# Kernel optimization log

Measured on AMD Instinct MI355X. Metric: run time of the kernel, lower is better.

Reference implementation:

```python
import jax, jax.numpy as jnp
import numpy as np

B, T, D, H = 4, 2048, 512, 8
DH = D // H

def setup_inputs() -> dict:
    key = jax.random.key(0)
    k1, k2, k3, k4 = jax.random.split(key, 4)
    scale = 1.0 / np.sqrt(D)
    return {
        "x": jax.random.normal(k1, (B, T, D), dtype=jnp.float32),
        "attn_mask": jnp.ones((B, T), dtype=jnp.int32),
        "bias": jax.random.normal(k2, (B, T, T), dtype=jnp.float32),
        "W_qkv": jax.random.normal(k3, (D, 3 * D), dtype=jnp.float32) * scale,
        "W_out": jax.random.normal(k4, (D, D), dtype=jnp.float32) * scale,
    }

def reference(x, attn_mask, bias, W_qkv, W_out):
    qkv = x @ W_qkv                      # [B,T,3D]
    q, k, v = jnp.split(qkv, 3, axis=-1)
    def heads(t):                        # [B,T,D] -> [B,H,T,DH]
        return t.reshape(B, T, H, DH).transpose(0, 2, 1, 3)
    q, k, v = heads(q), heads(k), heads(v)
    logits = jnp.einsum('bhqd,bhkd->bhqk', q, k) / np.sqrt(DH)
    logits = logits + bias[:, None, :, :]
    mask = (attn_mask[:, None, None, :] != 0)
    logits = jnp.where(mask, logits, -jnp.inf)
    attn = jax.nn.softmax(logits, axis=-1)
    out = jnp.einsum('bhqk,bhkd->bhqd', attn, v)  # [B,H,T,DH]
    out = out.transpose(0, 2, 1, 3).reshape(B, T, D)
    return out @ W_out
```

## Files before the change

kernel.cpp:

```cpp
#include <hip/hip_runtime.h>
#include <hip/hip_bf16.h>
#include <stdint.h>

#define Bc 4
#define Tc 2048
#define Dc 512
#define Hc 8

typedef __bf16 bf16x8 __attribute__((ext_vector_type(8)));
typedef float  f32x4  __attribute__((ext_vector_type(4)));
typedef unsigned short u16x8 __attribute__((ext_vector_type(8)));

__device__ __forceinline__ unsigned short f2b(float f) {
  union { float f; unsigned u; } v; v.f = f;
  unsigned r = v.u + 0x7fffu + ((v.u >> 16) & 1u);
  return (unsigned short)(r >> 16);
}

__device__ __forceinline__ unsigned short f2b_native(float f) {
  __bf16 b = (__bf16)f;
  return __builtin_bit_cast(unsigned short, b);
}

__device__ __forceinline__ bf16x8 ld_frag(const unsigned short* p) {
  u16x8 u = *(const u16x8*)p;
  return __builtin_bit_cast(bf16x8, u);
}

__device__ __forceinline__ void gload_lds16(const unsigned short* g, unsigned short* l) {
  __builtin_amdgcn_global_load_lds((const __attribute__((address_space(1))) void*)g,
                                   (__attribute__((address_space(3))) void*)l,
                                   16, 0, 0);
}

__global__ __launch_bounds__(256) void cvt_bf16(const float* __restrict__ in,
                                                unsigned short* __restrict__ out, int n) {
  int i = (blockIdx.x * 256 + threadIdx.x) * 8;
  if (i >= n) return;
  float4 a = *(const float4*)&in[i];
  float4 b = *(const float4*)&in[i + 4];
  u16x8 r;
  r[0] = f2b(a.x); r[1] = f2b(a.y); r[2] = f2b(a.z); r[3] = f2b(a.w);
  r[4] = f2b(b.x); r[5] = f2b(b.y); r[6] = f2b(b.z); r[7] = f2b(b.w);
  *(u16x8*)&out[i] = r;
}

__global__ __launch_bounds__(256) void transp_bf16(const float* __restrict__ in,
                                                   unsigned short* __restrict__ out,
                                                   int R, int C) {
  __shared__ float tile[32][33];
  int c0 = blockIdx.x * 32, r0 = blockIdx.y * 32;
  int lx = threadIdx.x & 31, ly = threadIdx.x >> 5;
  #pragma unroll
  for (int i = 0; i < 32; i += 8) tile[ly + i][lx] = in[(size_t)(r0 + ly + i) * C + c0 + lx];
  __syncthreads();
  #pragma unroll
  for (int i = 0; i < 32; i += 8) out[(size_t)(c0 + ly + i) * R + r0 + lx] = f2b(tile[lx][ly + i]);
}

__global__ __launch_bounds__(256) void transp_v(const unsigned short* __restrict__ qkv,
                                                unsigned short* __restrict__ vtg) {
  __shared__ unsigned short tile[32][34];
  int t0 = blockIdx.x * 32;
  int d0 = blockIdx.y * 32;
  int b  = blockIdx.z;
  int lx = threadIdx.x & 31, ly = threadIdx.x >> 5;
  #pragma unroll
  for (int i = 0; i < 32; i += 8)
    tile[ly + i][lx] = qkv[(size_t)(b * Tc + t0 + ly + i) * 1536 + 1024 + d0 + lx];
  __syncthreads();
  #pragma unroll
  for (int i = 0; i < 32; i += 8)
    vtg[(size_t)(b * 512 + d0 + ly + i) * Tc + t0 + lx] = tile[lx][ly + i];
}

template <int N, int OUTF32>
__global__ __launch_bounds__(256) void gemm_bt(const unsigned short* __restrict__ A,
                                               const unsigned short* __restrict__ Bt,
                                               void* __restrict__ Cout, int M, int K) {
  __shared__ unsigned short As[128 * 32];
  __shared__ unsigned short Bs[128 * 32];
  const int tid = threadIdx.x;
  const int lane = tid & 63;
  const int wid = tid >> 6;
  const int wm = (wid >> 1) * 64;
  const int wn = (wid & 1) * 64;
  const int m0 = blockIdx.x * 128;
  const int n0 = blockIdx.y * 128;
  const int l15 = lane & 15;
  const int lg = lane >> 4;

  f32x4 acc[4][4];
  #pragma unroll
  for (int i = 0; i < 4; i++)
    #pragma unroll
    for (int j = 0; j < 4; j++) acc[i][j] = (f32x4){0.f, 0.f, 0.f, 0.f};

  const int srow = tid >> 2;
  const int scol = (tid & 3) * 8;

  for (int k0 = 0; k0 < K; k0 += 32) {
    __syncthreads();
    gload_lds16(&A[(size_t)(m0 + srow) * K + k0 + scol],      &As[tid * 8]);
    gload_lds16(&A[(size_t)(m0 + 64 + srow) * K + k0 + scol], &As[2048 + tid * 8]);
    gload_lds16(&Bt[(size_t)(n0 + srow) * K + k0 + scol],      &Bs[tid * 8]);
    gload_lds16(&Bt[(size_t)(n0 + 64 + srow) * K + k0 + scol], &Bs[2048 + tid * 8]);
    __syncthreads();
    bf16x8 af[4], bfr[4];
    #pragma unroll
    for (int m = 0; m < 4; m++) af[m] = ld_frag(&As[(wm + m * 16 + l15) * 32 + lg * 8]);
    #pragma unroll
    for (int n = 0; n < 4; n++) bfr[n] = ld_frag(&Bs[(wn + n * 16 + l15) * 32 + lg * 8]);
    #pragma unroll
    for (int m = 0; m < 4; m++)
      #pragma unroll
      for (int n = 0; n < 4; n++)
        acc[m][n] = __builtin_amdgcn_mfma_f32_16x16x32_bf16(af[m], bfr[n], acc[m][n], 0, 0, 0);
  }

  #pragma unroll
  for (int m = 0; m < 4; m++)
    #pragma unroll
    for (int n = 0; n < 4; n++)
      #pragma unroll
      for (int j = 0; j < 4; j++) {
        int row = m0 + wm + m * 16 + lg * 4 + j;
        int col = n0 + wn + n * 16 + l15;
        float v = acc[m][n][j];
        if (OUTF32) ((float*)Cout)[(size_t)row * N + col] = v;
        else ((unsigned short*)Cout)[(size_t)row * N + col] = f2b(v);
      }
}

__global__ __launch_bounds__(256, 5) void attn_kernel(const unsigned short* __restrict__ qkv,
                                                      const unsigned short* __restrict__ vtg,
                                                      const float* __restrict__ bias,
                                                      const int* __restrict__ amask,
                                                      unsigned short* __restrict__ ctx) {
  __shared__ unsigned short Ks[64 * 64];
  __shared__ unsigned short Vs[64 * 64];
  __shared__ unsigned short Pt[4][16 * 72];

  const int NQ = Tc / 64;
  const int bid = blockIdx.x;
  const int b = bid / (Hc * NQ);
  const int h = (bid / NQ) % Hc;
  const int q0 = (bid % NQ) * 64;
  const int tid = threadIdx.x;
  const int lane = tid & 63;
  const int w = tid >> 6;
  const int l15 = lane & 15;
  const int lg = lane >> 4;

  const float LOG2E = 1.44269504f;

  const int qrow = q0 + w * 16 + l15;
  const size_t qoff = (size_t)(b * Tc + qrow) * 1536 + h * 64;
  bf16x8 qf0 = ld_frag(&qkv[qoff + lg * 8]);
  bf16x8 qf1 = ld_frag(&qkv[qoff + 32 + lg * 8]);

  u16x8 ou;
  #pragma unroll
  for (int e = 0; e < 8; e++) ou[e] = 0x3f80;
  const bf16x8 ones = __builtin_bit_cast(bf16x8, ou);

  f32x4 o[4];
  f32x4 osum = (f32x4){0.f, 0.f, 0.f, 0.f};
  #pragma unroll
  for (int n = 0; n < 4; n++) o[n] = (f32x4){0.f, 0.f, 0.f, 0.f};

  const int skey = tid >> 3;
  const int sc = tid & 7;
  const int sgc = sc ^ (skey & 7);

  const size_t kcol = (size_t)b * Tc * 1536 + 512 + h * 64;
  const unsigned short* vrow = &vtg[(size_t)(b * 512 + h * 64) * Tc];

  const float* bq = bias + (size_t)(b * Tc + q0 + w * 16 + l15) * Tc;
  const int* mq = amask + b * Tc;

  unsigned short* ptw = &Pt[w][0];

  for (int kt = 0; kt < Tc; kt += 64) {
    __syncthreads();
    {
      const size_t kbase = kcol + (size_t)kt * 1536;
      gload_lds16(&qkv[kbase + (size_t)skey * 1536 + sgc * 8],        &Ks[tid * 8]);
      gload_lds16(&qkv[kbase + (size_t)(skey + 32) * 1536 + sgc * 8], &Ks[2048 + tid * 8]);
      gload_lds16(&vrow[(size_t)skey * Tc + kt + sgc * 8],        &Vs[tid * 8]);
      gload_lds16(&vrow[(size_t)(skey + 32) * Tc + kt + sgc * 8], &Vs[2048 + tid * 8]);
    }
    float bf_[4][4];
    #pragma unroll
    for (int t2 = 0; t2 < 4; t2++) {
      float4 bb = *(const float4*)&bq[kt + t2 * 16 + lg * 4];
      int4 mm = *(const int4*)&mq[kt + t2 * 16 + lg * 4];
      bf_[t2][0] = mm.x ? bb.x * LOG2E : -1e30f;
      bf_[t2][1] = mm.y ? bb.y * LOG2E : -1e30f;
      bf_[t2][2] = mm.z ? bb.z * LOG2E : -1e30f;
      bf_[t2][3] = mm.w ? bb.w * LOG2E : -1e30f;
    }
    __syncthreads();

    f32x4 s[4];
    #pragma unroll
    for (int t2 = 0; t2 < 4; t2++) {
      int key = t2 * 16 + l15;
      bf16x8 kb0 = ld_frag(&Ks[key * 64 + ((lg) ^ (key & 7)) * 8]);
      bf16x8 kb1 = ld_frag(&Ks[key * 64 + ((4 + lg) ^ (key & 7)) * 8]);
      f32x4 z = (f32x4){0.f, 0.f, 0.f, 0.f};
      z = __builtin_amdgcn_mfma_f32_16x16x32_bf16(kb0, qf0, z, 0, 0, 0);
      z = __builtin_amdgcn_mfma_f32_16x16x32_bf16(kb1, qf1, z, 0, 0, 0);
      s[t2] = z;
    }

    #pragma unroll
    for (int t2 = 0; t2 < 4; t2++)
      #pragma unroll
      for (int j = 0; j < 4; j++)
        s[t2][j] = exp2f(fmaf(s[t2][j], 0.125f * LOG2E, bf_[t2][j]));

    #pragma unroll
    for (int t2 = 0; t2 < 4; t2++) {
      ushort4 pw;
      pw.x = f2b_native(s[t2][0]);
      pw.y = f2b_native(s[t2][1]);
      pw.z = f2b_native(s[t2][2]);
      pw.w = f2b_native(s[t2][3]);
      *(ushort4*)&ptw[l15 * 72 + t2 * 16 + lg * 4] = pw;
    }

    #pragma unroll
    for (int ks = 0; ks < 2; ks++) {
      bf16x8 pa = ld_frag(&ptw[l15 * 72 + ks * 32 + lg * 8]);
      osum = __builtin_amdgcn_mfma_f32_16x16x32_bf16(pa, ones, osum, 0, 0, 0);
      #pragma unroll
      for (int n = 0; n < 4; n++) {
        int d = n * 16 + l15;
        bf16x8 vb = ld_frag(&Vs[d * 64 + ((ks * 4 + lg) ^ (d & 7)) * 8]);
        o[n] = __builtin_amdgcn_mfma_f32_16x16x32_bf16(pa, vb, o[n], 0, 0, 0);
      }
    }
  }

  #pragma unroll
  for (int n = 0; n < 4; n++)
    #pragma unroll
    for (int j = 0; j < 4; j++) {
      int q = q0 + w * 16 + lg * 4 + j;
      ctx[(size_t)(b * Tc + q) * Dc + h * 64 + n * 16 + l15] = f2b(o[n][j] / osum[j]);
    }
}

extern "C" void kernel_launch(void* const* d_in, const int* in_sizes, int n_in,
                              void* d_out, int out_size, void* d_ws, size_t ws_size,
                              hipStream_t stream) {
  const float* x     = (const float*)d_in[0];
  const int*   amask = (const int*)d_in[1];
  const float* bias  = (const float*)d_in[2];
  const float* Wqkv  = (const float*)d_in[3];
  const float* Wout  = (const float*)d_in[4];
  float* out = (float*)d_out;
  char* ws = (char*)d_ws;

  unsigned short* xb    = (unsigned short*)(ws + 0);
  unsigned short* wqkvT = (unsigned short*)(ws + 8388608);
  unsigned short* woutT = (unsigned short*)(ws + 9961472);
  unsigned short* qkv   = (unsigned short*)(ws + 10485760);
  unsigned short* ctx   = (unsigned short*)(ws + 35651584);
  unsigned short* vtg   = (unsigned short*)(ws + 44040192);

  cvt_bf16<<<2048, 256, 0, stream>>>(x, xb, Bc * Tc * Dc);
  transp_bf16<<<dim3(48, 16), 256, 0, stream>>>(Wqkv, wqkvT, 512, 1536);
  transp_bf16<<<dim3(16, 16), 256, 0, stream>>>(Wout, woutT, 512, 512);
  gemm_bt<1536, 0><<<dim3(64, 12), 256, 0, stream>>>(xb, wqkvT, (void*)qkv, 8192, 512);
  transp_v<<<dim3(64, 16, 4), 256, 0, stream>>>(qkv, vtg);
  attn_kernel<<<1024, 256, 0, stream>>>(qkv, vtg, bias, amask, ctx);
  gemm_bt<512, 1><<<dim3(64, 4), 256, 0, stream>>>(ctx, woutT, (void*)out, 8192, 512);
}
```

Baseline: 158.8 us.

## Process 32 query rows per wave to reuse K/V tiles across two groups

Each attention block now covers 128 query rows instead of 64. Each wave handles two 16-row groups that share the same K and V fragments loaded from LDS, so every K/V tile staged in shared memory feeds twice as many MFMAs and K/V global traffic is halved. The launch drops to 512 blocks, which is only about two blocks per CU on the MI355X. The occupancy hint is removed, and s_setprio is raised around the MFMA sections. The costs are more registers per thread and fewer waves available to hide latency.

```diff
diff --git a/kernel.cpp b/kernel.cpp
--- a/kernel.cpp
+++ b/kernel.cpp
@@ -132,20 +132,20 @@
       }
 }
 
-__global__ __launch_bounds__(256, 5) void attn_kernel(const unsigned short* __restrict__ qkv,
-                                                      const unsigned short* __restrict__ vtg,
-                                                      const float* __restrict__ bias,
-                                                      const int* __restrict__ amask,
-                                                      unsigned short* __restrict__ ctx) {
+__global__ __launch_bounds__(256) void attn_kernel(const unsigned short* __restrict__ qkv,
+                                                   const unsigned short* __restrict__ vtg,
+                                                   const float* __restrict__ bias,
+                                                   const int* __restrict__ amask,
+                                                   unsigned short* __restrict__ ctx) {
   __shared__ unsigned short Ks[64 * 64];
   __shared__ unsigned short Vs[64 * 64];
-  __shared__ unsigned short Pt[4][16 * 72];
-
-  const int NQ = Tc / 64;
+  __shared__ unsigned short Pt[4][32 * 78];
+
+  const int NQ = Tc / 128;
   const int bid = blockIdx.x;
   const int b = bid / (Hc * NQ);
   const int h = (bid / NQ) % Hc;
-  const int q0 = (bid % NQ) * 64;
+  const int q0 = (bid % NQ) * 128;
   const int tid = threadIdx.x;
   const int lane = tid & 63;
   const int w = tid >> 6;
@@ -153,21 +153,30 @@
   const int lg = lane >> 4;
 
   const float LOG2E = 1.44269504f;
-
-  const int qrow = q0 + w * 16 + l15;
-  const size_t qoff = (size_t)(b * Tc + qrow) * 1536 + h * 64;
-  bf16x8 qf0 = ld_frag(&qkv[qoff + lg * 8]);
-  bf16x8 qf1 = ld_frag(&qkv[qoff + 32 + lg * 8]);
+  const float SC = 0.125f * LOG2E;
+
+  bf16x8 qf[2][2];
+  #pragma unroll
+  for (int g = 0; g < 2; g++) {
+    const int qrow = q0 + w * 32 + g * 16 + l15;
+    const size_t qoff = (size_t)(b * Tc + qrow) * 1536 + h * 64;
+    qf[g][0] = ld_frag(&qkv[qoff + lg * 8]);
+    qf[g][1] = ld_frag(&qkv[qoff + 32 + lg * 8]);
+  }
 
   u16x8 ou;
   #pragma unroll
   for (int e = 0; e < 8; e++) ou[e] = 0x3f80;
   const bf16x8 ones = __builtin_bit_cast(bf16x8, ou);
 
-  f32x4 o[4];
-  f32x4 osum = (f32x4){0.f, 0.f, 0.f, 0.f};
-  #pragma unroll
-  for (int n = 0; n < 4; n++) o[n] = (f32x4){0.f, 0.f, 0.f, 0.f};
+  f32x4 o[2][4];
+  f32x4 osum[2];
+  #pragma unroll
+  for (int g = 0; g < 2; g++) {
+    osum[g] = (f32x4){0.f, 0.f, 0.f, 0.f};
+    #pragma unroll
+    for (int n = 0; n < 4; n++) o[g][n] = (f32x4){0.f, 0.f, 0.f, 0.f};
+  }
 
   const int skey = tid >> 3;
   const int sc = tid & 7;
@@ -176,7 +185,10 @@
   const size_t kcol = (size_t)b * Tc * 1536 + 512 + h * 64;
   const unsigned short* vrow = &vtg[(size_t)(b * 512 + h * 64) * Tc];
 
-  const float* bq = bias + (size_t)(b * Tc + q0 + w * 16 + l15) * Tc;
+  const float* bq[2];
+  #pragma unroll
+  for (int g = 0; g < 2; g++)
+    bq[g] = bias + (size_t)(b * Tc + q0 + w * 32 + g * 16 + l15) * Tc;
   const int* mq = amask + b * Tc;
 
   unsigned short* ptw = &Pt[w][0];
@@ -190,66 +202,85 @@
       gload_lds16(&vrow[(size_t)skey * Tc + kt + sgc * 8],        &Vs[tid * 8]);
       gload_lds16(&vrow[(size_t)(skey + 32) * Tc + kt + sgc * 8], &Vs[2048 + tid * 8]);
     }
-    float bf_[4][4];
+    float bf_[2][4][4];
     #pragma unroll
     for (int t2 = 0; t2 < 4; t2++) {
-      float4 bb = *(const float4*)&bq[kt + t2 * 16 + lg * 4];
       int4 mm = *(const int4*)&mq[kt + t2 * 16 + lg * 4];
-      bf_[t2][0] = mm.x ? bb.x * LOG2E : -1e30f;
-      bf_[t2][1] = mm.y ? bb.y * LOG2E : -1e30f;
-      bf_[t2][2] = mm.z ? bb.z * LOG2E : -1e30f;
-      bf_[t2][3] = mm.w ? bb.w * LOG2E : -1e30f;
+      float m0 = mm.x ? 0.f : -1e30f;
+      float m1 = mm.y ? 0.f : -1e30f;
+      float m2 = mm.z ? 0.f : -1e30f;
+      float m3 = mm.w ? 0.f : -1e30f;
+      #pragma unroll
+      for (int g = 0; g < 2; g++) {
+        float4 bb = *(const float4*)&bq[g][kt + t2 * 16 + lg * 4];
+        bf_[g][t2][0] = fmaf(bb.x, LOG2E, m0);
+        bf_[g][t2][1] = fmaf(bb.y, LOG2E, m1);
+        bf_[g][t2][2] = fmaf(bb.z, LOG2E, m2);
+        bf_[g][t2][3] = fmaf(bb.w, LOG2E, m3);
+      }
     }
     __syncthreads();
 
-    f32x4 s[4];
+    f32x4 s[2][4];
+    __builtin_amdgcn_s_setprio(1);
     #pragma unroll
     for (int t2 = 0; t2 < 4; t2++) {
-      int key = t2 * 16 + l15;
+      const int key = t2 * 16 + l15;
       bf16x8 kb0 = ld_frag(&Ks[key * 64 + ((lg) ^ (key & 7)) * 8]);
       bf16x8 kb1 = ld_frag(&Ks[key * 64 + ((4 + lg) ^ (key & 7)) * 8]);
-      f32x4 z = (f32x4){0.f, 0.f, 0.f, 0.f};
-      z = __builtin_amdgcn_mfma_f32_16x16x32_bf16(kb0, qf0, z, 0, 0, 0);
-      z = __builtin_amdgcn_mfma_f32_16x16x32_bf16(kb1, qf1, z, 0, 0, 0);
-      s[t2] = z;
-    }
-
-    #pragma unroll
-    for (int t2 = 0; t2 < 4; t2++)
-      #pragma unroll
-      for (int j = 0; j < 4; j++)
-        s[t2][j] = exp2f(fmaf(s[t2][j], 0.125f * LOG2E, bf_[t2][j]));
-
-    #pragma unroll
-    for (int t2 = 0; t2 < 4; t2++) {
-      ushort4 pw;
-      pw.x = f2b_native(s[t2][0]);
-      pw.y = f2b_native(s[t2][1]);
-      pw.z = f2b_native(s[t2][2]);
-      pw.w = f2b_native(s[t2][3]);
-      *(ushort4*)&ptw[l15 * 72 + t2 * 16 + lg * 4] = pw;
-    }
-
+      #pragma unroll
+      for (int g = 0; g < 2; g++) {
+        f32x4 z = (f32x4){0.f, 0.f, 0.f, 0.f};
+        z = __builtin_amdgcn_mfma_f32_16x16x32_bf16(kb0, qf[g][0], z, 0, 0, 0);
+        z = __builtin_amdgcn_mfma_f32_16x16x32_bf16(kb1, qf[g][1], z, 0, 0, 0);
+        s[g][t2] = z;
+      }
+    }
+    __builtin_amdgcn_s_setprio(0);
+
+    #pragma unroll
+    for (int g = 0; g < 2; g++) {
+      #pragma unroll
+      for (int t2 = 0; t2 < 4; t2++) {
+        #pragma unroll
+        for (int j = 0; j < 4; j++)
+          s[g][t2][j] = exp2f(fmaf(s[g][t2][j], SC, bf_[g][t2][j]));
+        ushort4 pw;
+        pw.x = f2b_native(s[g][t2][0]);
+        pw.y = f2b_native(s[g][t2][1]);
+        pw.z = f2b_native(s[g][t2][2]);
+        pw.w = f2b_native(s[g][t2][3]);
+        *(ushort4*)&ptw[(g * 16 + l15) * 78 + t2 * 16 + lg * 4] = pw;
+      }
+    }
+
+    __builtin_amdgcn_s_setprio(1);
     #pragma unroll
     for (int ks = 0; ks < 2; ks++) {
-      bf16x8 pa = ld_frag(&ptw[l15 * 72 + ks * 32 + lg * 8]);
-      osum = __builtin_amdgcn_mfma_f32_16x16x32_bf16(pa, ones, osum, 0, 0, 0);
+      bf16x8 pa0 = ld_frag(&ptw[(0 * 16 + l15) * 78 + ks * 32 + lg * 8]);
+      bf16x8 pa1 = ld_frag(&ptw[(1 * 16 + l15) * 78 + ks * 32 + lg * 8]);
+      osum[0] = __builtin_amdgcn_mfma_f32_16x16x32_bf16(pa0, ones, osum[0], 0, 0, 0);
+      osum[1] = __builtin_amdgcn_mfma_f32_16x16x32_bf16(pa1, ones, osum[1], 0, 0, 0);
       #pragma unroll
       for (int n = 0; n < 4; n++) {
-        int d = n * 16 + l15;
+        const int d = n * 16 + l15;
         bf16x8 vb = ld_frag(&Vs[d * 64 + ((ks * 4 + lg) ^ (d & 7)) * 8]);
-        o[n] = __builtin_amdgcn_mfma_f32_16x16x32_bf16(pa, vb, o[n], 0, 0, 0);
-      }
-    }
+        o[0][n] = __builtin_amdgcn_mfma_f32_16x16x32_bf16(pa0, vb, o[0][n], 0, 0, 0);
+        o[1][n] = __builtin_amdgcn_mfma_f32_16x16x32_bf16(pa1, vb, o[1][n], 0, 0, 0);
+      }
+    }
+    __builtin_amdgcn_s_setprio(0);
   }
 
   #pragma unroll
-  for (int n = 0; n < 4; n++)
-    #pragma unroll
-    for (int j = 0; j < 4; j++) {
-      int q = q0 + w * 16 + lg * 4 + j;
-      ctx[(size_t)(b * Tc + q) * Dc + h * 64 + n * 16 + l15] = f2b(o[n][j] / osum[j]);
-    }
+  for (int g = 0; g < 2; g++)
+    #pragma unroll
+    for (int n = 0; n < 4; n++)
+      #pragma unroll
+      for (int j = 0; j < 4; j++) {
+        int q = q0 + w * 32 + g * 16 + lg * 4 + j;
+        ctx[(size_t)(b * Tc + q) * Dc + h * 64 + n * 16 + l15] = f2b(o[g][n][j] / osum[g][j]);
+      }
 }
 
 extern "C" void kernel_launch(void* const* d_in, const int* in_sizes, int n_in,
@@ -275,6 +306,6 @@
   transp_bf16<<<dim3(16, 16), 256, 0, stream>>>(Wout, woutT, 512, 512);
   gemm_bt<1536, 0><<<dim3(64, 12), 256, 0, stream>>>(xb, wqkvT, (void*)qkv, 8192, 512);
   transp_v<<<dim3(64, 16, 4), 256, 0, stream>>>(qkv, vtg);
-  attn_kernel<<<1024, 256, 0, stream>>>(qkv, vtg, bias, amask, ctx);
+  attn_kernel<<<512, 256, 0, stream>>>(qkv, vtg, bias, amask, ctx);
   gemm_bt<512, 1><<<dim3(64, 4), 256, 0, stream>>>(ctx, woutT, (void*)out, 8192, 512);
 }
```

Measured after the change: 180.0 us. 13.3% more time.

## Swizzle P tile in LDS, pack bf16 converts, add MFMA priority hints

Applied to the files above, without the earlier changes.

The P staging buffer moves from a padded 72-stride layout to an XOR-swizzled 64-stride layout. This trims LDS use and avoids bank conflicts on the write and fragment-read paths. Float-to-bf16 conversion now uses the packed v_cvt_pk_bf16_f32 instruction, and s_setprio raises wave priority around the two MFMA phases. The min-blocks launch bound of 5 is dropped, which lets the compiler use more registers but may lower occupancy.

```diff
diff --git a/kernel.cpp b/kernel.cpp
--- a/kernel.cpp
+++ b/kernel.cpp
@@ -17,11 +17,6 @@
   return (unsigned short)(r >> 16);
 }
 
-__device__ __forceinline__ unsigned short f2b_native(float f) {
-  __bf16 b = (__bf16)f;
-  return __builtin_bit_cast(unsigned short, b);
-}
-
 __device__ __forceinline__ bf16x8 ld_frag(const unsigned short* p) {
   u16x8 u = *(const u16x8*)p;
   return __builtin_bit_cast(bf16x8, u);
@@ -31,6 +26,12 @@
   __builtin_amdgcn_global_load_lds((const __attribute__((address_space(1))) void*)g,
                                    (__attribute__((address_space(3))) void*)l,
                                    16, 0, 0);
+}
+
+__device__ __forceinline__ unsigned cvtpk_bf16(float lo, float hi) {
+  unsigned r;
+  asm("v_cvt_pk_bf16_f32 %0, %1, %2" : "=v"(r) : "v"(lo), "v"(hi));
+  return r;
 }
 
 __global__ __launch_bounds__(256) void cvt_bf16(const float* __restrict__ in,
@@ -132,14 +133,14 @@
       }
 }
 
-__global__ __launch_bounds__(256, 5) void attn_kernel(const unsigned short* __restrict__ qkv,
-                                                      const unsigned short* __restrict__ vtg,
-                                                      const float* __restrict__ bias,
-                                                      const int* __restrict__ amask,
-                                                      unsigned short* __restrict__ ctx) {
+__global__ __launch_bounds__(256) void attn_kernel(const unsigned short* __restrict__ qkv,
+                                                   const unsigned short* __restrict__ vtg,
+                                                   const float* __restrict__ bias,
+                                                   const int* __restrict__ amask,
+                                                   unsigned short* __restrict__ ctx) {
   __shared__ unsigned short Ks[64 * 64];
   __shared__ unsigned short Vs[64 * 64];
-  __shared__ unsigned short Pt[4][16 * 72];
+  __shared__ unsigned short Pt[4][16 * 64];
 
   const int NQ = Tc / 64;
   const int bid = blockIdx.x;
@@ -153,6 +154,7 @@
   const int lg = lane >> 4;
 
   const float LOG2E = 1.44269504f;
+  const float SC = 0.125f * LOG2E;
 
   const int qrow = q0 + w * 16 + l15;
   const size_t qoff = (size_t)(b * Tc + qrow) * 1536 + h * 64;
@@ -203,6 +205,7 @@
     __syncthreads();
 
     f32x4 s[4];
+    __builtin_amdgcn_s_setprio(1);
     #pragma unroll
     for (int t2 = 0; t2 < 4; t2++) {
       int key = t2 * 16 + l15;
@@ -213,26 +216,24 @@
       z = __builtin_amdgcn_mfma_f32_16x16x32_bf16(kb1, qf1, z, 0, 0, 0);
       s[t2] = z;
     }
-
-    #pragma unroll
-    for (int t2 = 0; t2 < 4; t2++)
+    __builtin_amdgcn_s_setprio(0);
+
+    #pragma unroll
+    for (int t2 = 0; t2 < 4; t2++) {
       #pragma unroll
       for (int j = 0; j < 4; j++)
-        s[t2][j] = exp2f(fmaf(s[t2][j], 0.125f * LOG2E, bf_[t2][j]));
-
-    #pragma unroll
-    for (int t2 = 0; t2 < 4; t2++) {
-      ushort4 pw;
-      pw.x = f2b_native(s[t2][0]);
-      pw.y = f2b_native(s[t2][1]);
-      pw.z = f2b_native(s[t2][2]);
-      pw.w = f2b_native(s[t2][3]);
-      *(ushort4*)&ptw[l15 * 72 + t2 * 16 + lg * 4] = pw;
-    }
-
+        s[t2][j] = exp2f(fmaf(s[t2][j], SC, bf_[t2][j]));
+      uint2 pw;
+      pw.x = cvtpk_bf16(s[t2][0], s[t2][1]);
+      pw.y = cvtpk_bf16(s[t2][2], s[t2][3]);
+      const int cp = (2 * t2 + (lg >> 1)) ^ (l15 & 7);
+      *(uint2*)&ptw[l15 * 64 + cp * 8 + (lg & 1) * 4] = pw;
+    }
+
+    __builtin_amdgcn_s_setprio(1);
     #pragma unroll
     for (int ks = 0; ks < 2; ks++) {
-      bf16x8 pa = ld_frag(&ptw[l15 * 72 + ks * 32 + lg * 8]);
+      bf16x8 pa = ld_frag(&ptw[l15 * 64 + ((ks * 4 + lg) ^ (l15 & 7)) * 8]);
       osum = __builtin_amdgcn_mfma_f32_16x16x32_bf16(pa, ones, osum, 0, 0, 0);
       #pragma unroll
       for (int n = 0; n < 4; n++) {
@@ -241,6 +242,7 @@
         o[n] = __builtin_amdgcn_mfma_f32_16x16x32_bf16(pa, vb, o[n], 0, 0, 0);
       }
     }
+    __builtin_amdgcn_s_setprio(0);
   }
 
   #pragma unroll
```

Measured after the change: 167.4 us. 5.4% more time.
